# Kernel tuning notes

Measured on AMD Instinct MI355X. Metric: run time of the kernel, lower is better.

Reference implementation:

```python
import jax, jax.numpy as jnp
import numpy as np

N_DIM = 8
NUM_GRID = 2 ** N_DIM  # 256 local lattice offsets


def _e8_basis_param():
    # nn.Parameter init: E8 generator matrix / 2
    b = np.array([
        [2, 0, 0, 0, 0, 0, 0, 0],
        [0, 2, 0, 0, 0, 0, 0, 0],
        [0, 0, 2, 0, 0, 0, 0, 0],
        [0, 0, 0, 2, 0, 0, 0, 0],
        [1, 1, 1, 0, 1, 0, 0, 0],
        [1, 0, 1, 1, 0, 1, 0, 0],
        [1, 0, 0, 1, 1, 0, 1, 0],
        [1, 0, 0, 0, 1, 1, 0, 1],
    ], dtype=np.float32) / 2.0
    return jnp.asarray(b)


def _make_grid():
    # torch.cartesian_prod of [0,1]*N: first dim varies slowest
    j = jnp.arange(NUM_GRID)[:, None]
    shifts = jnp.arange(N_DIM - 1, -1, -1)[None, :]
    return ((j >> shifts) & 1).astype(jnp.float32)  # [256, 8]


def _normalized_basis(basis_param):
    b = jnp.tril(basis_param)
    det = jnp.prod(jnp.diagonal(b))  # triangular -> product of diagonal
    return b / jnp.abs(det)


def _find_nearest(x, basis, grid):
    B, K = x.shape
    # sequential triangular basis reduction (static unroll over N=8 dims)
    us = []
    x_temp = x
    for i in range(N_DIM)[::-1]:
        ui = jnp.floor(x_temp[:, i] / basis[i, i])  # [B]
        us.append(ui)
        if i != 0:
            x_temp = x_temp[:, :i] - ui[:, None] * basis[i, :i][None, :]
    dot = jnp.stack(us[::-1], axis=1)  # [B, N]
    pts = dot[:, None, :] + grid[None, :, :]  # [B, 256, N]
    code_book = jnp.einsum('bjn,nk->bjk', pts, basis)  # [B, 256, K]
    # squared l2 distance: ||x||^2 + ||cb||^2 - 2 cb.x
    dist = (jnp.sum(x * x, axis=1)[:, None]
            + jnp.sum(code_book * code_book, axis=2)
            - 2.0 * jnp.einsum('bjk,bk->bj', code_book, x)) / K  # [B, 256]
    idx = jnp.argmin(dist, axis=-1)  # [B]
    # one-hot scatter + einsum combine == gather of nearest codeword
    x_hat = jnp.take_along_axis(code_book, idx[:, None, None], axis=1)[:, 0, :]
    return x_hat, dist


def setup_inputs() -> dict:
    key = jax.random.key(0)
    kx, = jax.random.split(key, 1)
    B = 131072
    x = jax.random.normal(kx, (B, N_DIM), dtype=jnp.float32)
    basis_param = _e8_basis_param()
    return {"x": x, "basis_param": basis_param, "training": 0}


def reference(x, basis_param, training):
    basis = _normalized_basis(basis_param)
    grid = _make_grid()
    x_hat, dist = _find_nearest(x, basis, grid)
    # eval path: return (x_hat, x_indexes, dist) with x_indexes == x_hat
    return (x_hat, x_hat, dist)
```

## Files before the change

kernel.cpp:

```cpp
#include <hip/hip_runtime.h>
#include <hip/hip_bf16.h>
#include <cstdint>

#define WAVES 4

typedef float fx4 __attribute__((ext_vector_type(4)));

__global__ __launch_bounds__(256) void lvq_main(
    const float* __restrict__ x,
    const float* __restrict__ bp,
    float* __restrict__ oxh0,
    float* __restrict__ oxh1,
    float* __restrict__ odist,
    int B)
{
    __shared__ __align__(16) float sbasis[8][8];
    __shared__ __align__(16) float sgrid[256][8];
    __shared__ __align__(16) float scg2[256];
    __shared__ __align__(16) fx4 sbufv[WAVES][64][8];

    const int tid  = threadIdx.x;
    const int lane = tid & 63;
    const int wid  = tid >> 6;

    if (tid < 64) {
        const int i = tid >> 3, k = tid & 7;
        float det = 1.f;
        #pragma unroll
        for (int d = 0; d < 8; ++d) det *= bp[d * 8 + d];
        const float ad = fabsf(det);
        sbasis[i][k] = (k <= i) ? (bp[i * 8 + k] / ad) : 0.f;
    }
    __syncthreads();

    {
        const int j = tid;
        float g[8];
        #pragma unroll
        for (int k = 0; k < 8; ++k) {
            float s = 0.f;
            #pragma unroll
            for (int n = 0; n < 8; ++n)
                if ((j >> (7 - n)) & 1) s += sbasis[n][k];
            g[k] = s;
            sgrid[j][k] = s;
        }
        float g2 = 0.f;
        #pragma unroll
        for (int k = 0; k < 8; ++k) g2 += g[k] * g[k];
        int t = j; t ^= t >> 1; t ^= t >> 2; t ^= t >> 4;
        scg2[t] = g2 * 0.125f;
    }
    __syncthreads();

    const int group = blockIdx.x * WAVES + wid;
    const int b0 = group * 64;
    if (b0 >= B) return;
    const int b = b0 + lane;

    const float4* xp = reinterpret_cast<const float4*>(x + (size_t)b * 8);
    const float4 xa = xp[0], xb_ = xp[1];
    float xv[8] = {xa.x, xa.y, xa.z, xa.w, xb_.x, xb_.y, xb_.z, xb_.w};

    float xt[8];
    #pragma unroll
    for (int k = 0; k < 8; ++k) xt[k] = xv[k];
    float r[8];
    #pragma unroll
    for (int i = 7; i >= 0; --i) {
        const float bii = sbasis[i][i];
        const float ui = floorf(xt[i] / bii);
        r[i] = xt[i] - ui * bii;
        #pragma unroll
        for (int k = 0; k < i; ++k) xt[k] -= ui * sbasis[i][k];
    }
    float C = 0.f;
    #pragma unroll
    for (int k = 0; k < 8; ++k) C += r[k] * r[k];
    C *= 0.125f;
    float w[8];
    #pragma unroll
    for (int k = 0; k < 8; ++k) w[k] = -0.25f * r[k];
    float bnw[8];
    #pragma unroll
    for (int n = 0; n < 8; ++n) {
        float s = 0.f;
        #pragma unroll
        for (int k = 0; k <= n; ++k) s += sbasis[n][k] * w[k];
        bnw[n] = s;
    }

    float acc = 0.f;
    float md = 3.4e38f;
    int jmin = 0;
    const int g = lane & 7, K = lane >> 3;

    for (int c = 0; c < 8; ++c) {
        if (c) {
            const int p2 = __builtin_ctz(c);
            const float delta = (p2 == 0) ? bnw[2] : ((p2 == 1) ? bnw[1] : bnw[0]);
            const int gb = ((c ^ (c >> 1)) >> p2) & 1;
            acc = gb ? (acc + delta) : (acc - delta);
        }
        const int jb   = (c ^ (c >> 1)) << 5;
        const int fix4 = (c & 1) << 4;
        const int fix2 = (c & 1) << 2;
        const float bn3s = (c & 1) ? -bnw[3] : bnw[3];

        #pragma unroll
        for (int m = 0; m < 8; ++m) {
            const float4 c4 = *reinterpret_cast<const float4*>(&scg2[c * 32 + m * 4]);
            const float cg[4] = {c4.x, c4.y, c4.z, c4.w};
            float va[4];
            #pragma unroll
            for (int s = 0; s < 4; ++s) {
                const int tp = 4 * m + s;
                if (tp == 16) {
                    acc += bn3s;
                } else if (tp > 0) {
                    const int p = __builtin_ctz(tp);
                    const int sgn = ((tp ^ (tp >> 1)) >> p) & 1;
                    const int n = 7 - p;
                    acc = sgn ? (acc + bnw[n]) : (acc - bnw[n]);
                }
                const float d = (C + cg[tp & 3]) + acc;
                const int slot2 = (s ^ (s >> 1)) ^ ((m & 1) << 1);
                va[slot2] = d;
                const int jlow = ((tp ^ (tp >> 1)) & 15) | (tp & 16);
                const int j = jb ^ fix4 ^ jlow;
                if (d < md) { md = d; jmin = j; }
            }
            const int Q = (m & 4) | ((m ^ (m >> 1)) & 3);
            fx4 v4;
            v4.x = va[0]; v4.y = va[1]; v4.z = va[2]; v4.w = va[3];
            sbufv[wid][lane][Q ^ (lane & 7)] = v4;
        }
        const fx4* lsrc = &sbufv[wid][K][(g ^ fix2) ^ K];
        fx4* gdst = reinterpret_cast<fx4*>(odist + (size_t)(b0 + K) * 256 + jb) + g;
        #pragma unroll
        for (int it = 0; it < 8; ++it) {
            __builtin_nontemporal_store(lsrc[it * 64], &gdst[it * 512]);
        }
    }

    const float4 ga = *reinterpret_cast<const float4*>(&sgrid[jmin][0]);
    const float4 gb2 = *reinterpret_cast<const float4*>(&sgrid[jmin][4]);
    const float gm[8] = {ga.x, ga.y, ga.z, ga.w, gb2.x, gb2.y, gb2.z, gb2.w};
    float xh[8];
    #pragma unroll
    for (int k = 0; k < 8; ++k) xh[k] = (xv[k] - r[k]) + gm[k];
    const float4 h0 = make_float4(xh[0], xh[1], xh[2], xh[3]);
    const float4 h1 = make_float4(xh[4], xh[5], xh[6], xh[7]);
    reinterpret_cast<float4*>(oxh0 + (size_t)b * 8)[0] = h0;
    reinterpret_cast<float4*>(oxh0 + (size_t)b * 8)[1] = h1;
    reinterpret_cast<float4*>(oxh1 + (size_t)b * 8)[0] = h0;
    reinterpret_cast<float4*>(oxh1 + (size_t)b * 8)[1] = h1;
}

extern "C" void kernel_launch(void* const* d_in, const int* in_sizes, int n_in,
                              void* d_out, int out_size, void* d_ws, size_t ws_size,
                              hipStream_t stream) {
    const float* x  = (const float*)d_in[0];
    const float* bp = (const float*)d_in[1];
    const int B = in_sizes[0] / 8;
    float* out   = (float*)d_out;
    float* oxh0  = out;
    float* oxh1  = out + (size_t)B * 8;
    float* odist = out + (size_t)2 * B * 8;
    const int groups = (B + 63) / 64;
    const int blocks = (groups + WAVES - 1) / WAVES;
    lvq_main<<<blocks, 256, 0, stream>>>(x, bp, oxh0, oxh1, odist, B);
}
```

Baseline: 34.28 us.

## Compute distance rows directly per lane instead of staging through LDS transpose

The distance matrix is now written by a separate pass. Each lane broadcasts its per-row coefficients (C and the basis-weighted terms) through shared memory. The wave then computes four adjacent columns of every row with FMAs and stores full contiguous rows. The Gray-code loop keeps only the argmin. This removes the LDS staging buffer and its swizzled transpose stores, but it adds a second full pass of arithmetic, a block-wide barrier, and plain stores in place of nontemporal ones. Distance values are also summed in a different order than the argmin path, so tie-breaking could differ slightly.

New measurement: 31.36 us. -8.5%, faster.

```diff
diff --git a/kernel.cpp b/kernel.cpp
--- a/kernel.cpp
+++ b/kernel.cpp
@@ -17,7 +17,8 @@
     __shared__ __align__(16) float sbasis[8][8];
     __shared__ __align__(16) float sgrid[256][8];
     __shared__ __align__(16) float scg2[256];
-    __shared__ __align__(16) fx4 sbufv[WAVES][64][8];
+    __shared__ __align__(16) float scg2lin[256];
+    __shared__ __align__(16) float sprow[WAVES][64][12];
 
     const int tid  = threadIdx.x;
     const int lane = tid & 63;
@@ -50,6 +51,7 @@
         for (int k = 0; k < 8; ++k) g2 += g[k] * g[k];
         int t = j; t ^= t >> 1; t ^= t >> 2; t ^= t >> 4;
         scg2[t] = g2 * 0.125f;
+        scg2lin[j] = g2 * 0.125f;
     }
     __syncthreads();
 
@@ -90,10 +92,50 @@
         bnw[n] = s;
     }
 
+    {
+        fx4 q0; q0.x = C;      q0.y = bnw[0]; q0.z = bnw[1]; q0.w = bnw[2];
+        fx4 q1; q1.x = bnw[3]; q1.y = bnw[4]; q1.z = bnw[5]; q1.w = bnw[6];
+        *reinterpret_cast<fx4*>(&sprow[wid][lane][0]) = q0;
+        *reinterpret_cast<fx4*>(&sprow[wid][lane][4]) = q1;
+        sprow[wid][lane][8] = bnw[7];
+    }
+    __syncthreads();
+
+    {
+        float fb[6];
+        #pragma unroll
+        for (int n = 0; n < 6; ++n) fb[n] = (float)((lane >> (5 - n)) & 1);
+        const fx4 cgv = *reinterpret_cast<const fx4*>(&scg2lin[4 * lane]);
+
+        float* orow = odist + (size_t)b0 * 256;
+        #pragma unroll 8
+        for (int rr = 0; rr < 64; ++rr) {
+            const fx4 a  = *reinterpret_cast<const fx4*>(&sprow[wid][rr][0]);
+            const fx4 bq = *reinterpret_cast<const fx4*>(&sprow[wid][rr][4]);
+            const float b7 = sprow[wid][rr][8];
+            float base = a.x;
+            base = fmaf(fb[0], a.y, base);
+            base = fmaf(fb[1], a.z, base);
+            base = fmaf(fb[2], a.w, base);
+            base = fmaf(fb[3], bq.x, base);
+            base = fmaf(fb[4], bq.y, base);
+            base = fmaf(fb[5], bq.z, base);
+            const float t7  = base + b7;
+            const float t6  = base + bq.w;
+            const float t67 = t6 + b7;
+            fx4 v;
+            v.x = base + cgv.x;
+            v.y = t7  + cgv.y;
+            v.z = t6  + cgv.z;
+            v.w = t67 + cgv.w;
+            fx4* gdst = reinterpret_cast<fx4*>(orow + (size_t)rr * 256);
+            gdst[lane] = v;
+        }
+    }
+
     float acc = 0.f;
     float md = 3.4e38f;
     int jmin = 0;
-    const int g = lane & 7, K = lane >> 3;
 
     for (int c = 0; c < 8; ++c) {
         if (c) {
@@ -104,14 +146,12 @@
         }
         const int jb   = (c ^ (c >> 1)) << 5;
         const int fix4 = (c & 1) << 4;
-        const int fix2 = (c & 1) << 2;
         const float bn3s = (c & 1) ? -bnw[3] : bnw[3];
 
         #pragma unroll
         for (int m = 0; m < 8; ++m) {
             const float4 c4 = *reinterpret_cast<const float4*>(&scg2[c * 32 + m * 4]);
             const float cg[4] = {c4.x, c4.y, c4.z, c4.w};
-            float va[4];
             #pragma unroll
             for (int s = 0; s < 4; ++s) {
                 const int tp = 4 * m + s;
@@ -124,22 +164,10 @@
                     acc = sgn ? (acc + bnw[n]) : (acc - bnw[n]);
                 }
                 const float d = (C + cg[tp & 3]) + acc;
-                const int slot2 = (s ^ (s >> 1)) ^ ((m & 1) << 1);
-                va[slot2] = d;
                 const int jlow = ((tp ^ (tp >> 1)) & 15) | (tp & 16);
                 const int j = jb ^ fix4 ^ jlow;
                 if (d < md) { md = d; jmin = j; }
             }
-            const int Q = (m & 4) | ((m ^ (m >> 1)) & 3);
-            fx4 v4;
-            v4.x = va[0]; v4.y = va[1]; v4.z = va[2]; v4.w = va[3];
-            sbufv[wid][lane][Q ^ (lane & 7)] = v4;
-        }
-        const fx4* lsrc = &sbufv[wid][K][(g ^ fix2) ^ K];
-        fx4* gdst = reinterpret_cast<fx4*>(odist + (size_t)(b0 + K) * 256 + jb) + g;
-        #pragma unroll
-        for (int it = 0; it < 8; ++it) {
-            __builtin_nontemporal_store(lsrc[it * 64], &gdst[it * 512]);
         }
     }
 
```
